# Optimization experiments

Measured on AMD Instinct MI355X. Metric: run time of the kernel, lower is better.

Reference implementation:

```python
import jax, jax.numpy as jnp
import numpy as np

B, S, HID = 4, 2048, 1024
NH, IM, E = 4, 2048, 4
EPS = 1e-6


def setup_inputs() -> dict:
    key = jax.random.key(0)
    ks = jax.random.split(key, 12)
    init = lambda k, shape: (jax.random.normal(k, shape, jnp.float32) * 0.02)
    return {
        "hidden_states": jax.random.normal(ks[0], (B, S, HID), jnp.float32),
        "ln1_w": jnp.ones((HID,), jnp.float32),
        "wq": init(ks[1], (HID, HID)),
        "wk": init(ks[2], (HID, HID)),
        "wv": init(ks[3], (HID, HID)),
        "wo": init(ks[4], (HID, HID)),
        "ln2_w": jnp.ones((HID,), jnp.float32),
        "router_w": init(ks[5], (HID, E)),
        "router_b": jnp.zeros((E,), jnp.float32),
        "gate_w": init(ks[6], (E, HID, IM)),
        "up_w": init(ks[7], (E, HID, IM)),
        "down_w": init(ks[8], (E, IM, HID)),
    }


def _rms(x, w):
    return w * (x * jax.lax.rsqrt(jnp.mean(x * x, axis=-1, keepdims=True) + EPS))


def reference(hidden_states, ln1_w, wq, wk, wv, wo, ln2_w,
              router_w, router_b, gate_w, up_w, down_w):
    b, s, h = hidden_states.shape
    nh, d = NH, h // NH

    # ---- attention block (elu+1 feature map, then full softmax) ----
    x = _rms(hidden_states, ln1_w)
    q = (x @ wq).reshape(b, s, nh, d).transpose(0, 2, 1, 3)  # [b,nh,s,d]
    k = (x @ wk).reshape(b, s, nh, d).transpose(0, 2, 1, 3)
    v = (x @ wv).reshape(b, s, nh, d).transpose(0, 2, 1, 3)
    q = jax.nn.elu(q) + 1.0
    k = jax.nn.elu(k) + 1.0
    scores = jnp.einsum('bhqd,bhkd->bhqk', q, k)
    attn = jax.nn.softmax(scores, axis=-1)  # dropout is identity at eval
    o = jnp.einsum('bhqk,bhkd->bhqd', attn, v)
    o = o.transpose(0, 2, 1, 3).reshape(b, s, h) @ wo
    h1 = hidden_states + o

    # ---- MoE block: router softmax, balance loss, dense expert loop ----
    x2 = _rms(h1, ln2_w)
    logits = x2 @ router_w + router_b            # [b,s,E]
    rw = jax.nn.softmax(logits, axis=-1)
    mean_routing = rw.mean(axis=0)               # mean over batch dim only, [s,E]
    balance_loss = jnp.mean((mean_routing - 1.0 / E) ** 2) * 0.01

    # source computes EVERY expert over all tokens, weighted by the FULL
    # softmax routing weight (top-k weights are computed but unused)
    moe_out = jnp.zeros_like(x2)
    for i in range(E):
        g = jax.nn.silu(x2 @ gate_w[i])
        u = x2 @ up_w[i]
        moe_out = moe_out + ((g * u) @ down_w[i]) * rw[..., i:i + 1]

    return h1 + moe_out, balance_loss
```

## Files before the change

### kernel.cpp

```cpp
#include <hip/hip_runtime.h>
#include <cstdint>
#include <cstddef>

#define B_    4
#define S_    2048
#define HID_  1024
#define NH_   4
#define HD_   256
#define IM_   2048
#define E_    4
#define M_    8192
#define NHG_  4

typedef __bf16 bf16x8 __attribute__((ext_vector_type(8)));
typedef float  f32x4  __attribute__((ext_vector_type(4)));

__device__ __forceinline__ unsigned short f32_to_bf16(float f) {
  unsigned int u = __float_as_uint(f);
  u += 0x7fffu + ((u >> 16) & 1u);
  return (unsigned short)(u >> 16);
}

__device__ __forceinline__ void gload16(const unsigned short* g, unsigned short* l) {
  __builtin_amdgcn_global_load_lds(
      (const __attribute__((address_space(1))) void*)g,
      (__attribute__((address_space(3))) void*)l, 16, 0, 0);
}

template<int N> __device__ __forceinline__ void vwait() {
  if constexpr (N == 0)      asm volatile("s_waitcnt vmcnt(0)" ::: "memory");
  else if constexpr (N == 2) asm volatile("s_waitcnt vmcnt(2)" ::: "memory");
  else if constexpr (N == 6) asm volatile("s_waitcnt vmcnt(6)" ::: "memory");
  else                       asm volatile("s_waitcnt vmcnt(8)" ::: "memory");
}
__device__ __forceinline__ void lgk0() {
  asm volatile("s_waitcnt lgkmcnt(0)" ::: "memory");
}

__device__ __forceinline__ void swizzle_xy(int& bx, int& by) {
  const int gx = gridDim.x, gy = gridDim.y;
  const int flat = blockIdx.x + blockIdx.y * gx;
  const int xcd = flat & 7, i = flat >> 3;
  const int rpx = gy >> 3;
  bx = i % gx;
  by = xcd * rpx + i / gx;
}

#define EPI_F32      0
#define EPI_VT       2
#define EPI_PV_O     3
#define EPI_WO       4
#define EPI_DOWN     5

struct EpiAux {
  float* c_f32;
  unsigned short* c_bf16;
  const float* add_src;
  float* out2;
  long long strideCz;
  int ldc;
};

template<int EPI>
__global__ __launch_bounds__(256) void gemm_bf16k(
    const unsigned short* __restrict__ A, int lda, long long sAo, long long sAi, int zbA,
    const unsigned short* __restrict__ B, int ldb, long long sBo, long long sBi, int zbB,
    int zshift, int zmask, int zbC, int K, EpiAux aux)
{
  __shared__ unsigned short As[2][128 * 32];
  __shared__ unsigned short Bs[2][128 * 32];

  const int t = threadIdx.x;
  int bx, by;
  swizzle_xy(bx, by);
  const int m0 = by * 128, n0 = bx * 128;
  const int z  = blockIdx.z;
  const int zA = z + zbA, zB = z + zbB, zC = z + zbC;
  const unsigned short* Ab = A + (long long)(zA >> zshift) * sAo + (long long)(zA & zmask) * sAi;
  const unsigned short* Bb = B + (long long)(zB >> zshift) * sBo + (long long)(zB & zmask) * sBi;

  const int lane = t & 63, wave = t >> 6;
  const int wm = (wave >> 1) * 64, wn = (wave & 1) * 64;
  const int lrow = lane & 15, quad = lane >> 4;

  f32x4 acc[4][4] = {};

  const int srow = lane >> 2;
  const int sko  = (lane & 3) * 8;
  const unsigned short* aRow0 = Ab + (long long)(m0 + wave * 16       + srow) * lda + sko;
  const unsigned short* aRow1 = Ab + (long long)(m0 + (wave + 4) * 16 + srow) * lda + sko;
  const unsigned short* bRow0 = Bb + (long long)(n0 + wave * 16       + srow) * ldb + sko;
  const unsigned short* bRow1 = Bb + (long long)(n0 + (wave + 4) * 16 + srow) * ldb + sko;
  const int dst0 = (wave * 16) * 32, dst1 = ((wave + 4) * 16) * 32;

  gload16(aRow0, &As[0][dst0]);
  gload16(aRow1, &As[0][dst1]);
  gload16(bRow0, &Bs[0][dst0]);
  gload16(bRow1, &Bs[0][dst1]);

  int cur = 0;
  for (int kk = 0; kk < K; kk += 32, cur ^= 1) {
    __syncthreads();
    if (kk + 32 < K) {
      const int nxt = cur ^ 1, k2 = kk + 32;
      gload16(aRow0 + k2, &As[nxt][dst0]);
      gload16(aRow1 + k2, &As[nxt][dst1]);
      gload16(bRow0 + k2, &Bs[nxt][dst0]);
      gload16(bRow1 + k2, &Bs[nxt][dst1]);
    }
    bf16x8 af[4], bfr[4];
    #pragma unroll
    for (int i = 0; i < 4; ++i) {
      af[i]  = *reinterpret_cast<const bf16x8*>(&As[cur][(wm + i * 16 + lrow) * 32 + quad * 8]);
      bfr[i] = *reinterpret_cast<const bf16x8*>(&Bs[cur][(wn + i * 16 + lrow) * 32 + quad * 8]);
    }
    #pragma unroll
    for (int i = 0; i < 4; ++i)
      #pragma unroll
      for (int j = 0; j < 4; ++j)
        acc[i][j] = __builtin_amdgcn_mfma_f32_16x16x32_bf16(af[i], bfr[j], acc[i][j], 0, 0, 0);
  }

  #pragma unroll
  for (int mi = 0; mi < 4; ++mi) {
    #pragma unroll
    for (int ni = 0; ni < 4; ++ni) {
      #pragma unroll
      for (int r = 0; r < 4; ++r) {
        const int gm = m0 + wm + mi * 16 + quad * 4 + r;
        const int gn = n0 + wn + ni * 16 + lrow;
        const float val = acc[mi][ni][r];
        if (EPI == EPI_F32) {
          aux.c_f32[(long long)zC * aux.strideCz + (long long)gm * aux.ldc + gn] = val;
        } else if (EPI == EPI_VT) {
          const int b = gm >> 11, s = gm & (S_ - 1);
          const int h = gn >> 8, d = gn & (HD_ - 1);
          aux.c_bf16[((long long)(b * NH_ + h) * HD_ + d) * S_ + s] = f32_to_bf16(val);
        } else if (EPI == EPI_PV_O) {
          const int b = zC >> 2, h = zC & (NH_ - 1);
          aux.c_bf16[((long long)(b * S_ + gm)) * HID_ + h * HD_ + gn] = f32_to_bf16(val);
        } else if (EPI == EPI_WO) {
          const long long idx = (long long)gm * HID_ + gn;
          aux.out2[idx] = val + aux.add_src[idx];
        } else if (EPI == EPI_DOWN) {
          const long long idx = (long long)gm * HID_ + gn;
          aux.out2[idx] += val;
        }
      }
    }
  }
}

#define EPI2_GU 1

template<int EPI2>
__global__ __launch_bounds__(256, 2) void gemm_dual_k(
    const unsigned short* __restrict__ A,
    const unsigned short* __restrict__ B0b,
    const unsigned short* __restrict__ B1b,
    int zb,
    unsigned short* __restrict__ out0, unsigned short* __restrict__ out1,
    const float* __restrict__ rw)
{
  __shared__ unsigned short As[2][128 * 32];
  __shared__ unsigned short B0s[2][128 * 32];
  __shared__ unsigned short B1s[2][128 * 32];

  const int t = threadIdx.x;
  int bx, by;
  swizzle_xy(bx, by);
  const int m0 = by * 128, n0 = bx * 128;

  const int lane = t & 63, wave = t >> 6;
  const int wm = (wave >> 1) * 64, wn = (wave & 1) * 64;
  const int lrow = lane & 15, quad = lane >> 4;

  f32x4 acc0[4][4] = {}, acc1[4][4] = {};

  const int srow = lane >> 2;
  const int sko  = (lane & 3) * 8;
  const unsigned short* aRow0 = A   + (long long)(m0 + wave * 16       + srow) * HID_ + sko;
  const unsigned short* aRow1 = A   + (long long)(m0 + (wave + 4) * 16 + srow) * HID_ + sko;
  const unsigned short* gRow0 = B0b + (long long)(n0 + wave * 16       + srow) * HID_ + sko;
  const unsigned short* gRow1 = B0b + (long long)(n0 + (wave + 4) * 16 + srow) * HID_ + sko;
  const unsigned short* uRow0 = B1b + (long long)(n0 + wave * 16       + srow) * HID_ + sko;
  const unsigned short* uRow1 = B1b + (long long)(n0 + (wave + 4) * 16 + srow) * HID_ + sko;
  const int dst0 = (wave * 16) * 32, dst1 = ((wave + 4) * 16) * 32;

  gload16(aRow0, &As[0][dst0]);
  gload16(aRow1, &As[0][dst1]);
  gload16(gRow0, &B0s[0][dst0]);
  gload16(gRow1, &B0s[0][dst1]);
  gload16(uRow0, &B1s[0][dst0]);
  gload16(uRow1, &B1s[0][dst1]);

  int cur = 0;
  for (int kk = 0; kk < HID_; kk += 32, cur ^= 1) {
    __syncthreads();
    if (kk + 32 < HID_) {
      const int nxt = cur ^ 1, k2 = kk + 32;
      gload16(aRow0 + k2, &As[nxt][dst0]);
      gload16(aRow1 + k2, &As[nxt][dst1]);
      gload16(gRow0 + k2, &B0s[nxt][dst0]);
      gload16(gRow1 + k2, &B0s[nxt][dst1]);
      gload16(uRow0 + k2, &B1s[nxt][dst0]);
      gload16(uRow1 + k2, &B1s[nxt][dst1]);
    }
    bf16x8 af[4], b0[4], b1[4];
    #pragma unroll
    for (int i = 0; i < 4; ++i) {
      af[i] = *reinterpret_cast<const bf16x8*>(&As[cur][(wm + i * 16 + lrow) * 32 + quad * 8]);
      b0[i] = *reinterpret_cast<const bf16x8*>(&B0s[cur][(wn + i * 16 + lrow) * 32 + quad * 8]);
      b1[i] = *reinterpret_cast<const bf16x8*>(&B1s[cur][(wn + i * 16 + lrow) * 32 + quad * 8]);
    }
    #pragma unroll
    for (int i = 0; i < 4; ++i)
      #pragma unroll
      for (int j = 0; j < 4; ++j) {
        acc0[i][j] = __builtin_amdgcn_mfma_f32_16x16x32_bf16(af[i], b0[j], acc0[i][j], 0, 0, 0);
        acc1[i][j] = __builtin_amdgcn_mfma_f32_16x16x32_bf16(af[i], b1[j], acc1[i][j], 0, 0, 0);
      }
  }

  #pragma unroll
  for (int mi = 0; mi < 4; ++mi)
    #pragma unroll
    for (int r = 0; r < 4; ++r) {
      const int gm = m0 + wm + mi * 16 + quad * 4 + r;
      const float rwv = rw[(long long)gm * E_ + zb];
      #pragma unroll
      for (int ni = 0; ni < 4; ++ni) {
        const int gn = n0 + wn + ni * 16 + lrow;
        const float v0 = acc0[mi][ni][r];
        const float v1 = acc1[mi][ni][r];
        const float sg = v0 / (1.f + __expf(-v0));
        out0[(long long)gm * IM_ + gn] = f32_to_bf16(sg * v1 * rwv);
      }
    }
}

#define EPI5_GU   0
#define EPI5_QK   1
#define EPI5_DOWN 2
#define EPI5_WO   3
template<bool DUAL, int EPI, int KTOT, int KROW, bool PAIRK>
__global__ __launch_bounds__(512, 2) void gemm5_k(
    const unsigned short* A0, const unsigned short* A1,
    const unsigned short* B0b, const unsigned short* B1b,
    const float* __restrict__ rw, int expert,
    unsigned short* out0, unsigned short* out1,
    float* o_f32, const float* add_src)
{
  constexpr int NT  = KTOT / 64;
  constexpr int NT2 = NT / 2;
  __shared__ unsigned short smem[DUAL ? 65536 : 57344];

  const int t = threadIdx.x, wave = t >> 6, lane = t & 63;
  const int lrow = lane & 15, quad = lane >> 4;
  const int wrow0 = (wave >> 1) * 64;
  const int wcol0 = (wave & 1) * 64;

  int bx, by;
  swizzle_xy(bx, by);
  const int m0 = by * 256, n0 = bx * 128;

  const int r8  = lane >> 3;
  const int csw = ((lane & 7) ^ r8) << 4;

  auto unit = [&](const unsigned short* mat, int grow0, int ktl, int ldsElem) {
    #pragma unroll
    for (int i = 0; i < 2; ++i) {
      const char* src = (const char*)(mat + (size_t)(grow0 + wave * 16 + i * 8 + r8) * KROW)
                        + (size_t)ktl * 128 + csw;
      gload16((const unsigned short*)src, &smem[ldsElem + wave * 1024 + i * 512]);
    }
  };
  auto stageA = [&](int kt) {
    const unsigned short* m = A0; int ktl = kt;
    if constexpr (PAIRK) { if (kt >= NT2) { m = A1; ktl = kt - NT2; } }
    const int buf = kt & 1;
    unit(m, m0,       ktl, buf * 16384);
    unit(m, m0 + 128, ktl, buf * 16384 + 8192);
  };
  auto stageB = [&](int kt, int which, int bufB) {
    const unsigned short* m; int ktl = kt;
    if constexpr (DUAL) {
      m = which ? B1b : B0b;
    } else {
      m = B0b;
      if constexpr (PAIRK) { if (kt >= NT2) { m = B1b; ktl = kt - NT2; } }
    }
    unit(m, n0, ktl, 32768 + (DUAL ? which * 16384 : 0) + bufB * 8192);
  };

  const int xr = (lane & 7) << 4;
  auto readA_ = [&](bf16x8* o, int buf, int ks) {
    const char* base = (const char*)smem + buf * 32768 + (wrow0 >> 7) * 16384;
    const int rl0 = wrow0 & 127;
    #pragma unroll
    for (int mi = 0; mi < 4; ++mi)
      o[mi] = *(const bf16x8*)(base + (rl0 + mi * 16 + lrow) * 128 + ((ks * 64 + quad * 16) ^ xr));
  };
  auto readB_ = [&](bf16x8* o, int baseByte, int ks) {
    const char* base = (const char*)smem + baseByte;
    #pragma unroll
    for (int nj = 0; nj < 4; ++nj)
      o[nj] = *(const bf16x8*)(base + (wcol0 + nj * 16 + lrow) * 128 + ((ks * 64 + quad * 16) ^ xr));
  };

  f32x4 acc0[4][4] = {};
  f32x4 acc1[4][4] = {};
  auto mm = [&](f32x4 (&ac)[4][4], const bf16x8* aF, const bf16x8* bF) {
    #pragma unroll
    for (int mi = 0; mi < 4; ++mi)
      #pragma unroll
      for (int nj = 0; nj < 4; ++nj)
        ac[mi][nj] = __builtin_amdgcn_mfma_f32_16x16x32_bf16(aF[mi], bF[nj], ac[mi][nj], 0, 0, 0);
  };

  bf16x8 a0[4], a1[4], bF[4];

  if constexpr (DUAL) {
    stageA(0); stageB(0, 1, 0); stageB(0, 0, 0); stageA(1); stageB(1, 1, 1);
    vwait<8>();
    __builtin_amdgcn_s_barrier();

    for (int T = 0; T < NT; ++T) {
      const int c = T & 1;
      const int bB1 = 65536 + 32768 + c * 16384;
      const int bB0 = 65536 + c * 16384;
      readA_(a0, c, 0);
      readB_(bF, bB1, 0);
      if (T + 1 < NT) stageB(T + 1, 0, (T + 1) & 1);
      if (T < NT - 1) vwait<8>(); else vwait<0>();
      __builtin_amdgcn_s_barrier();
      lgk0();
      __builtin_amdgcn_s_setprio(1); mm(acc1, a0, bF); __builtin_amdgcn_s_setprio(0);
      __builtin_amdgcn_s_barrier();
      readB_(bF, bB0, 0);
      __builtin_amdgcn_s_barrier();
      lgk0();
      __builtin_amdgcn_s_setprio(1); mm(acc0, a0, bF); __builtin_amdgcn_s_setprio(0);
      __builtin_amdgcn_s_barrier();
      readA_(a1, c, 1);
      readB_(bF, bB1, 1);
      __builtin_amdgcn_s_barrier();
      lgk0();
      __builtin_amdgcn_s_setprio(1); mm(acc1, a1, bF); __builtin_amdgcn_s_setprio(0);
      __builtin_amdgcn_s_barrier();
      readB_(bF, bB0, 1);
      if (T + 2 < NT) { stageA(T + 2); stageB(T + 2, 1, c); }
      if (T < NT - 2) vwait<8>();
      else if (T == NT - 2) vwait<2>();
      __builtin_amdgcn_s_barrier();
      lgk0();
      __builtin_amdgcn_s_setprio(1); mm(acc0, a1, bF); __builtin_amdgcn_s_setprio(0);
      __builtin_amdgcn_s_barrier();
    }
  } else {
    stageB(0, 0, 0); stageA(0); stageB(1, 0, 1); stageA(1);
    vwait<6>();
    __builtin_amdgcn_s_barrier();

    int b = 0;
    for (int T = 0; T < NT; ++T) {
      const int c = T & 1;
      const int bB = 65536 + b * 16384;
      int bn = b + 2; if (bn >= 3) bn -= 3;
      readA_(a0, c, 0);
      readA_(a1, c, 1);
      readB_(bF, bB, 0);
      if (T + 2 < NT) stageB(T + 2, 0, bn);
      __builtin_amdgcn_s_barrier();
      lgk0();
      __builtin_amdgcn_s_setprio(1); mm(acc0, a0, bF); __builtin_amdgcn_s_setprio(0);
      __builtin_amdgcn_s_barrier();
      readB_(bF, bB, 1);
      if (T + 2 < NT) stageA(T + 2);
      if (T < NT - 2) vwait<6>();
      else if (T == NT - 2) vwait<0>();
      __builtin_amdgcn_s_barrier();
      lgk0();
      __builtin_amdgcn_s_setprio(1); mm(acc0, a1, bF); __builtin_amdgcn_s_setprio(0);
      __builtin_amdgcn_s_barrier();
      if (++b == 3) b = 0;
    }
  }

  #pragma unroll
  for (int mi = 0; mi < 4; ++mi) {
    #pragma unroll
    for (int r = 0; r < 4; ++r) {
      const int gm = m0 + wrow0 + mi * 16 + quad * 4 + r;
      float rwv = 0.f;
      if (EPI == EPI5_GU) rwv = rw[(size_t)gm * E_ + expert];
      #pragma unroll
      for (int nj = 0; nj < 4; ++nj) {
        const int gn = n0 + wcol0 + nj * 16 + lrow;
        const float v0 = acc0[mi][nj][r];
        if (EPI == EPI5_GU) {
          const float v1 = acc1[mi][nj][r];
          const float sg = v0 / (1.f + __expf(-v0));
          out0[(size_t)gm * IM_ + gn] = f32_to_bf16(sg * v1 * rwv);
        } else if (EPI == EPI5_QK) {
          const float v1 = acc1[mi][nj][r];
          out0[(size_t)gm * HID_ + gn] = f32_to_bf16(v0 > 0.f ? v0 + 1.f : __expf(v0));
          out1[(size_t)gm * HID_ + gn] = f32_to_bf16(v1 > 0.f ? v1 + 1.f : __expf(v1));
        } else if (EPI == EPI5_DOWN) {
          o_f32[(size_t)gm * HID_ + gn] += v0;
        } else {
          const size_t idx = (size_t)gm * HID_ + gn;
          o_f32[idx] = v0 + add_src[idx];
        }
      }
    }
  }
}

__global__ void transpose_cast4_k(const float* s0, const float* s1,
                                  const float* s2, const float* s3,
                                  unsigned short* __restrict__ out, int R, int C)
{
  __shared__ float tile[32][33];
  const int z = blockIdx.z;
  const float* in = (z == 0) ? s0 : (z == 1) ? s1 : (z == 2) ? s2 : s3;
  unsigned short* o = out + (long long)z * R * C;
  const int c0 = blockIdx.x * 32, r0 = blockIdx.y * 32;
  const int tx = threadIdx.x, ty = threadIdx.y;
  #pragma unroll
  for (int i = 0; i < 32; i += 8)
    tile[ty + i][tx] = in[(long long)(r0 + ty + i) * C + c0 + tx];
  __syncthreads();
  #pragma unroll
  for (int i = 0; i < 32; i += 8)
    o[(long long)(c0 + ty + i) * R + r0 + tx] = f32_to_bf16(tile[tx][ty + i]);
}

__global__ void transpose_cast2x4_k(const float* __restrict__ sA,
                                    const float* __restrict__ sB,
                                    unsigned short* __restrict__ dA,
                                    unsigned short* __restrict__ dB,
                                    int R, int C)
{
  __shared__ float tile[32][33];
  const int z = blockIdx.z;
  const long long eo = (long long)(z & 3) * R * C;
  const float* in = ((z < 4) ? sA : sB) + eo;
  unsigned short* o = ((z < 4) ? dA : dB) + eo;
  const int c0 = blockIdx.x * 32, r0 = blockIdx.y * 32;
  const int tx = threadIdx.x, ty = threadIdx.y;
  #pragma unroll
  for (int i = 0; i < 32; i += 8)
    tile[ty + i][tx] = in[(long long)(r0 + ty + i) * C + c0 + tx];
  __syncthreads();
  #pragma unroll
  for (int i = 0; i < 32; i += 8)
    o[(long long)(c0 + ty + i) * R + r0 + tx] = f32_to_bf16(tile[tx][ty + i]);
}

__global__ void transpose_cast_k(const float* __restrict__ in,
                                 unsigned short* __restrict__ out, int R, int C)
{
  __shared__ float tile[32][33];
  const long long bo = (long long)blockIdx.z * R * C;
  const int c0 = blockIdx.x * 32, r0 = blockIdx.y * 32;
  const int tx = threadIdx.x, ty = threadIdx.y;
  #pragma unroll
  for (int i = 0; i < 32; i += 8)
    tile[ty + i][tx] = in[bo + (long long)(r0 + ty + i) * C + c0 + tx];
  __syncthreads();
  #pragma unroll
  for (int i = 0; i < 32; i += 8)
    out[bo + (long long)(c0 + ty + i) * R + r0 + tx] = f32_to_bf16(tile[tx][ty + i]);
}

__global__ __launch_bounds__(256) void rmsnorm_cast_k(
    const float* __restrict__ x, const float* __restrict__ w,
    unsigned short* __restrict__ out)
{
  __shared__ float red[4];
  const int row = blockIdx.x, t = threadIdx.x;
  const float4 v = reinterpret_cast<const float4*>(x + (long long)row * HID_)[t];
  float ss = v.x * v.x + v.y * v.y + v.z * v.z + v.w * v.w;
  #pragma unroll
  for (int off = 32; off > 0; off >>= 1) ss += __shfl_down(ss, off, 64);
  if ((t & 63) == 0) red[t >> 6] = ss;
  __syncthreads();
  ss = red[0] + red[1] + red[2] + red[3];
  const float inv = rsqrtf(ss * (1.0f / HID_) + 1e-6f);
  const float4 wv = reinterpret_cast<const float4*>(w)[t];
  ushort4 o;
  o.x = f32_to_bf16(v.x * inv * wv.x);
  o.y = f32_to_bf16(v.y * inv * wv.y);
  o.z = f32_to_bf16(v.z * inv * wv.z);
  o.w = f32_to_bf16(v.w * inv * wv.w);
  reinterpret_cast<ushort4*>(out + (long long)row * HID_)[t] = o;
}

__global__ __launch_bounds__(256) void softmax_rows_k(float* __restrict__ scores)
{
  __shared__ float red[4];
  const long long rbase = ((long long)blockIdx.y * S_ + blockIdx.x) * S_;
  float* row = scores + rbase;
  const int t = threadIdx.x;
  float v[8];
  #pragma unroll
  for (int i = 0; i < 8; ++i) v[i] = row[t + i * 256];
  float m = v[0];
  #pragma unroll
  for (int i = 1; i < 8; ++i) m = fmaxf(m, v[i]);
  #pragma unroll
  for (int off = 32; off > 0; off >>= 1) m = fmaxf(m, __shfl_down(m, off, 64));
  if ((t & 63) == 0) red[t >> 6] = m;
  __syncthreads();
  m = fmaxf(fmaxf(red[0], red[1]), fmaxf(red[2], red[3]));
  __syncthreads();
  float s = 0.f;
  #pragma unroll
  for (int i = 0; i < 8; ++i) { v[i] = __expf(v[i] - m); s += v[i]; }
  #pragma unroll
  for (int off = 32; off > 0; off >>= 1) s += __shfl_down(s, off, 64);
  if ((t & 63) == 0) red[t >> 6] = s;
  __syncthreads();
  const float inv = 1.0f / (red[0] + red[1] + red[2] + red[3]);
  unsigned short* prow = reinterpret_cast<unsigned short*>(scores) + rbase * 2;
  #pragma unroll
  for (int i = 0; i < 8; ++i) prow[t + i * 256] = f32_to_bf16(v[i] * inv);
}

__global__ __launch_bounds__(256) void router_k(
    const float* __restrict__ h1, const float* __restrict__ ln2w,
    const float* __restrict__ rwgt, const float* __restrict__ rbias,
    float* __restrict__ rw)
{
  const int wv = threadIdx.x >> 6, lane = threadIdx.x & 63;
  const long long m = (long long)blockIdx.x * 4 + wv;
  const float* xr = h1 + m * HID_;
  float xv[16];
  float ss = 0.f;
  #pragma unroll
  for (int i = 0; i < 16; ++i) { xv[i] = xr[lane + i * 64]; ss += xv[i] * xv[i]; }
  #pragma unroll
  for (int off = 32; off > 0; off >>= 1) ss += __shfl_down(ss, off, 64);
  ss = __shfl(ss, 0, 64);
  const float inv = rsqrtf(ss * (1.0f / HID_) + 1e-6f);
  float l0 = 0, l1 = 0, l2 = 0, l3 = 0;
  #pragma unroll
  for (int i = 0; i < 16; ++i) {
    const int k = lane + i * 64;
    const float xn = xv[i] * inv * ln2w[k];
    const float4 wr = reinterpret_cast<const float4*>(rwgt)[k];
    l0 += xn * wr.x; l1 += xn * wr.y; l2 += xn * wr.z; l3 += xn * wr.w;
  }
  #pragma unroll
  for (int off = 32; off > 0; off >>= 1) {
    l0 += __shfl_down(l0, off, 64);
    l1 += __shfl_down(l1, off, 64);
    l2 += __shfl_down(l2, off, 64);
    l3 += __shfl_down(l3, off, 64);
  }
  if (lane == 0) {
    l0 += rbias[0]; l1 += rbias[1]; l2 += rbias[2]; l3 += rbias[3];
    const float mx = fmaxf(fmaxf(l0, l1), fmaxf(l2, l3));
    const float e0 = __expf(l0 - mx), e1 = __expf(l1 - mx);
    const float e2 = __expf(l2 - mx), e3 = __expf(l3 - mx);
    const float is = 1.0f / (e0 + e1 + e2 + e3);
    reinterpret_cast<float4*>(rw)[m] = make_float4(e0 * is, e1 * is, e2 * is, e3 * is);
  }
}

__global__ __launch_bounds__(256) void balance_k(const float* __restrict__ rw,
                                                 float* __restrict__ out_scalar)
{
  __shared__ float red[4];
  float acc = 0.f;
  for (int it = threadIdx.x; it < S_ * E_; it += 256) {
    const int s = it >> 2, e = it & 3;
    float mr = 0.f;
    #pragma unroll
    for (int b = 0; b < B_; ++b) mr += rw[((long long)b * S_ + s) * E_ + e];
    mr *= (1.0f / B_);
    const float d = mr - 1.0f / E_;
    acc += d * d;
  }
  #pragma unroll
  for (int off = 32; off > 0; off >>= 1) acc += __shfl_down(acc, off, 64);
  if ((threadIdx.x & 63) == 0) red[threadIdx.x >> 6] = acc;
  __syncthreads();
  if (threadIdx.x == 0)
    out_scalar[0] = (red[0] + red[1] + red[2] + red[3]) * (0.01f / (S_ * E_));
}

extern "C" void kernel_launch(void* const* d_in, const int* in_sizes, int n_in,
                              void* d_out, int out_size, void* d_ws, size_t ws_size,
                              hipStream_t stream)
{
  const float* hidden   = (const float*)d_in[0];
  const float* ln1w     = (const float*)d_in[1];
  const float* wq       = (const float*)d_in[2];
  const float* wk       = (const float*)d_in[3];
  const float* wv       = (const float*)d_in[4];
  const float* wo       = (const float*)d_in[5];
  const float* ln2w     = (const float*)d_in[6];
  const float* router_w = (const float*)d_in[7];
  const float* router_b = (const float*)d_in[8];
  const float* gate_w   = (const float*)d_in[9];
  const float* up_w     = (const float*)d_in[10];
  const float* down_w   = (const float*)d_in[11];
  float* out = (float*)d_out;

  char* ws = (char*)d_ws;
  size_t off = 0;
  auto carve = [&](size_t bytes) {
    off = (off + 255) & ~(size_t)255;
    char* p = ws + off;
    off += bytes;
    return p;
  };
  unsigned short* wqT   = (unsigned short*)carve((size_t)HID_ * HID_ * 2);
  unsigned short* wkT   = (unsigned short*)carve((size_t)HID_ * HID_ * 2);
  unsigned short* wvT   = (unsigned short*)carve((size_t)HID_ * HID_ * 2);
  unsigned short* woT   = (unsigned short*)carve((size_t)HID_ * HID_ * 2);
  unsigned short* x_bf  = (unsigned short*)carve((size_t)M_ * HID_ * 2);
  unsigned short* qb    = (unsigned short*)carve((size_t)M_ * HID_ * 2);
  unsigned short* kb    = (unsigned short*)carve((size_t)M_ * HID_ * 2);
  unsigned short* vT    = (unsigned short*)carve((size_t)M_ * HID_ * 2);
  float*          rwbuf = (float*)carve((size_t)M_ * E_ * 4);
  char*           ubase = carve((size_t)NHG_ * S_ * S_ * 4);
  float*          scores = (float*)ubase;
  unsigned short* gateT = (unsigned short*)(ubase);
  unsigned short* upT   = (unsigned short*)(ubase + (size_t)16 * 1024 * 1024);
  unsigned short* downT = (unsigned short*)(ubase + (size_t)32 * 1024 * 1024);
  unsigned short* o_bf  = x_bf;
  unsigned short* x2_bf = qb;
  unsigned short* gu0   = kb;
  unsigned short* gu1   = (unsigned short*)carve((size_t)M_ * IM_ * 2);
  const bool paired = (ws_size >= off);

  const dim3 blk256(256), blk512(512), blkT(32, 8);

  transpose_cast4_k<<<dim3(32, 32, 4), blkT, 0, stream>>>(wq, wk, wv, wo, wqT, HID_, HID_);

  rmsnorm_cast_k<<<M_, blk256, 0, stream>>>(hidden, ln1w, x_bf);

  gemm5_k<true, EPI5_QK, 1024, 1024, false><<<dim3(8, 32, 1), blk512, 0, stream>>>(
      x_bf, nullptr, wqT, wkT, nullptr, 0, qb, kb, nullptr, nullptr);
  {
    EpiAux a{}; a.c_bf16 = vT;
    gemm_bf16k<EPI_VT><<<dim3(8, 64, 1), blk256, 0, stream>>>(
        x_bf, HID_, 0, 0, 0, wvT, HID_, 0, 0, 0, 0, 0, 0, HID_, a);
  }

  for (int grp = 0; grp < 16 / NHG_; ++grp) {
    EpiAux as{}; as.c_f32 = scores; as.ldc = S_; as.strideCz = (long long)S_ * S_;
    gemm_bf16k<EPI_F32><<<dim3(16, 16, NHG_), blk256, 0, stream>>>(
        qb, HID_, (long long)S_ * HID_, HD_, grp * NHG_,
        kb, HID_, (long long)S_ * HID_, HD_, grp * NHG_,
        2, 3, 0, HD_, as);
    softmax_rows_k<<<dim3(S_, NHG_, 1), blk256, 0, stream>>>(scores);
    EpiAux ap{}; ap.c_bf16 = o_bf;
    gemm_bf16k<EPI_PV_O><<<dim3(2, 16, NHG_), blk256, 0, stream>>>(
        (const unsigned short*)scores, 2 * S_, (long long)S_ * 2 * S_, 0, 0,
        vT, S_, (long long)HD_ * S_, 0, grp * NHG_,
        0, 0, grp * NHG_, S_, ap);
  }

  transpose_cast2x4_k<<<dim3(64, 32, 8), blkT, 0, stream>>>(
      gate_w, up_w, gateT, upT, HID_, IM_);
  transpose_cast_k<<<dim3(32, 64, E_), blkT, 0, stream>>>(down_w, downT, IM_, HID_);

  gemm5_k<false, EPI5_WO, 1024, 1024, false><<<dim3(8, 32, 1), blk512, 0, stream>>>(
      o_bf, nullptr, woT, nullptr, nullptr, 0, nullptr, nullptr, out, hidden);

  rmsnorm_cast_k<<<M_, blk256, 0, stream>>>(out, ln2w, x2_bf);
  router_k<<<M_ / 4, blk256, 0, stream>>>(out, ln2w, router_w, router_b, rwbuf);
  balance_k<<<1, blk256, 0, stream>>>(rwbuf, out + (size_t)M_ * HID_);

  const size_t wsz = (size_t)IM_ * HID_;
  if (paired) {
    for (int p = 0; p < 2; ++p) {
      const int e0 = 2 * p, e1 = e0 + 1;
      gemm5_k<true, EPI5_GU, 1024, 1024, false><<<dim3(16, 32, 1), blk512, 0, stream>>>(
          x2_bf, nullptr, gateT + (size_t)e0 * wsz, upT + (size_t)e0 * wsz,
          rwbuf, e0, gu0, nullptr, nullptr, nullptr);
      gemm5_k<true, EPI5_GU, 1024, 1024, false><<<dim3(16, 32, 1), blk512, 0, stream>>>(
          x2_bf, nullptr, gateT + (size_t)e1 * wsz, upT + (size_t)e1 * wsz,
          rwbuf, e1, gu1, nullptr, nullptr, nullptr);
      gemm5_k<false, EPI5_DOWN, 4096, 2048, true><<<dim3(8, 32, 1), blk512, 0, stream>>>(
          gu0, gu1, downT + (size_t)e0 * wsz, downT + (size_t)e1 * wsz,
          nullptr, 0, nullptr, nullptr, out, nullptr);
    }
  } else {
    for (int i = 0; i < E_; ++i) {
      gemm_dual_k<EPI2_GU><<<dim3(16, 64, 1), blk256, 0, stream>>>(
          x2_bf, gateT + (size_t)i * wsz, upT + (size_t)i * wsz, i, gu0, nullptr, rwbuf);
      EpiAux ad{}; ad.out2 = out;
      gemm_bf16k<EPI_DOWN><<<dim3(8, 64, 1), blk256, 0, stream>>>(
          gu0, IM_, 0, 0, 0, downT + (size_t)i * wsz, IM_, 0, 0, 0,
          0, 0, 0, IM_, ad);
    }
  }
}
```

Baseline: 1.082 ms.

## Restructure GEMM prefetch pipeline with precomputed pointers and triple-buffered A

Rewrites the main MFMA GEMM kernel's load schedule. Global source pointers and LDS read offsets are now precomputed and advanced incrementally rather than recomputed per stage. The dual kernel reorders its MFMA phases and splits its A/B prefetches across phases. The single-B path now triple-buffers both A and B, which adds LDS (the shared array grows) to keep more loads in flight and cut address arithmetic and stalls in the pipeline. The higher LDS use may reduce occupancy, and the waitcnt accounting is more delicate.

Result: no change. 1.074 ms (-0.7%).

```diff
diff --git a/kernel.cpp b/kernel.cpp
--- a/kernel.cpp
+++ b/kernel.cpp
@@ -30,6 +30,7 @@
 template<int N> __device__ __forceinline__ void vwait() {
   if constexpr (N == 0)      asm volatile("s_waitcnt vmcnt(0)" ::: "memory");
   else if constexpr (N == 2) asm volatile("s_waitcnt vmcnt(2)" ::: "memory");
+  else if constexpr (N == 4) asm volatile("s_waitcnt vmcnt(4)" ::: "memory");
   else if constexpr (N == 6) asm volatile("s_waitcnt vmcnt(6)" ::: "memory");
   else                       asm volatile("s_waitcnt vmcnt(8)" ::: "memory");
 }
@@ -244,7 +245,7 @@
 #define EPI5_DOWN 2
 #define EPI5_WO   3
 template<bool DUAL, int EPI, int KTOT, int KROW, bool PAIRK>
-__global__ __launch_bounds__(512, 2) void gemm5_k(
+__global__ __launch_bounds__(512, 2) void gemm6_k(
     const unsigned short* A0, const unsigned short* A1,
     const unsigned short* B0b, const unsigned short* B1b,
     const float* __restrict__ rw, int expert,
@@ -253,7 +254,7 @@
 {
   constexpr int NT  = KTOT / 64;
   constexpr int NT2 = NT / 2;
-  __shared__ unsigned short smem[DUAL ? 65536 : 57344];
+  __shared__ unsigned short smem[DUAL ? 65536 : 73728];
 
   const int t = threadIdx.x, wave = t >> 6, lane = t & 63;
   const int lrow = lane & 15, quad = lane >> 4;
@@ -267,123 +268,147 @@
   const int r8  = lane >> 3;
   const int csw = ((lane & 7) ^ r8) << 4;
 
-  auto unit = [&](const unsigned short* mat, int grow0, int ktl, int ldsElem) {
+  const char* pA[4]; const char* qA[4];
+  const char* pB0[2]; const char* pB1[2];
+  #pragma unroll
+  for (int h = 0; h < 2; ++h)
     #pragma unroll
     for (int i = 0; i < 2; ++i) {
-      const char* src = (const char*)(mat + (size_t)(grow0 + wave * 16 + i * 8 + r8) * KROW)
-                        + (size_t)ktl * 128 + csw;
-      gload16((const unsigned short*)src, &smem[ldsElem + wave * 1024 + i * 512]);
+      const int row = m0 + h * 128 + wave * 16 + i * 8 + r8;
+      pA[h * 2 + i] = (const char*)(A0 + (size_t)row * KROW) + csw;
+      if constexpr (PAIRK) qA[h * 2 + i] = (const char*)(A1 + (size_t)row * KROW) + csw;
+    }
+  #pragma unroll
+  for (int i = 0; i < 2; ++i) {
+    const int row = n0 + wave * 16 + i * 8 + r8;
+    pB0[i] = (const char*)(B0b + (size_t)row * KROW) + csw;
+    if constexpr (DUAL || PAIRK) pB1[i] = (const char*)(B1b + (size_t)row * KROW) + csw;
+  }
+
+  const int dAe[4] = { wave * 1024, wave * 1024 + 512,
+                       8192 + wave * 1024, 8192 + wave * 1024 + 512 };
+  const int dBe[2] = { wave * 1024, wave * 1024 + 512 };
+
+  auto stA_h = [&](int h, int bufAel) {
+    #pragma unroll
+    for (int i = 0; i < 2; ++i) {
+      const int j = h * 2 + i;
+      gload16((const unsigned short*)pA[j], &smem[bufAel + dAe[j]]);
+      pA[j] += 128;
     }
   };
-  auto stageA = [&](int kt) {
-    const unsigned short* m = A0; int ktl = kt;
-    if constexpr (PAIRK) { if (kt >= NT2) { m = A1; ktl = kt - NT2; } }
-    const int buf = kt & 1;
-    unit(m, m0,       ktl, buf * 16384);
-    unit(m, m0 + 128, ktl, buf * 16384 + 8192);
+  auto stB_ = [&](const char** pB, int bel) {
+    #pragma unroll
+    for (int i = 0; i < 2; ++i) {
+      gload16((const unsigned short*)pB[i], &smem[bel + dBe[i]]);
+      pB[i] += 128;
+    }
   };
-  auto stageB = [&](int kt, int which, int bufB) {
-    const unsigned short* m; int ktl = kt;
-    if constexpr (DUAL) {
-      m = which ? B1b : B0b;
-    } else {
-      m = B0b;
-      if constexpr (PAIRK) { if (kt >= NT2) { m = B1b; ktl = kt - NT2; } }
-    }
-    unit(m, n0, ktl, 32768 + (DUAL ? which * 16384 : 0) + bufB * 8192);
+
+  const int xr = (lane & 7) << 4;
+  int roA[4], roB[4];
+  #pragma unroll
+  for (int mi = 0; mi < 4; ++mi)
+    roA[mi] = (wrow0 >> 7) * 16384 + ((wrow0 & 64) + mi * 16 + lrow) * 128
+              + ((quad * 16) ^ xr);
+  #pragma unroll
+  for (int nj = 0; nj < 4; ++nj)
+    roB[nj] = (wcol0 + nj * 16 + lrow) * 128 + ((quad * 16) ^ xr);
+
+  auto readA_ = [&](bf16x8* o, int aByte, int ks) {
+    const char* base = (const char*)smem + aByte;
+    #pragma unroll
+    for (int mi = 0; mi < 4; ++mi)
+      o[mi] = *(const bf16x8*)(base + (roA[mi] ^ (ks * 64)));
   };
-
-  const int xr = (lane & 7) << 4;
-  auto readA_ = [&](bf16x8* o, int buf, int ks) {
-    const char* base = (const char*)smem + buf * 32768 + (wrow0 >> 7) * 16384;
-    const int rl0 = wrow0 & 127;
-    #pragma unroll
-    for (int mi = 0; mi < 4; ++mi)
-      o[mi] = *(const bf16x8*)(base + (rl0 + mi * 16 + lrow) * 128 + ((ks * 64 + quad * 16) ^ xr));
-  };
-  auto readB_ = [&](bf16x8* o, int baseByte, int ks) {
-    const char* base = (const char*)smem + baseByte;
+  auto readB_ = [&](bf16x8* o, int bByte, int ks) {
+    const char* base = (const char*)smem + bByte;
     #pragma unroll
     for (int nj = 0; nj < 4; ++nj)
-      o[nj] = *(const bf16x8*)(base + (wcol0 + nj * 16 + lrow) * 128 + ((ks * 64 + quad * 16) ^ xr));
+      o[nj] = *(const bf16x8*)(base + (roB[nj] ^ (ks * 64)));
   };
 
   f32x4 acc0[4][4] = {};
   f32x4 acc1[4][4] = {};
-  auto mm = [&](f32x4 (&ac)[4][4], const bf16x8* aF, const bf16x8* bF) {
+  auto mm = [&](f32x4 (&ac)[4][4], const bf16x8* aF, const bf16x8* bFr) {
     #pragma unroll
     for (int mi = 0; mi < 4; ++mi)
       #pragma unroll
       for (int nj = 0; nj < 4; ++nj)
-        ac[mi][nj] = __builtin_amdgcn_mfma_f32_16x16x32_bf16(aF[mi], bF[nj], ac[mi][nj], 0, 0, 0);
+        ac[mi][nj] = __builtin_amdgcn_mfma_f32_16x16x32_bf16(aF[mi], bFr[nj], ac[mi][nj], 0, 0, 0);
   };
 
   bf16x8 a0[4], a1[4], bF[4];
 
   if constexpr (DUAL) {
-    stageA(0); stageB(0, 1, 0); stageB(0, 0, 0); stageA(1); stageB(1, 1, 1);
-    vwait<8>();
+    stA_h(0, 0); stA_h(1, 0);
+    stB_(pB0, 32768); stB_(pB1, 49152);
+    stA_h(0, 16384); stA_h(1, 16384);
+    vwait<4>();
     __builtin_amdgcn_s_barrier();
 
     for (int T = 0; T < NT; ++T) {
-      const int c = T & 1;
-      const int bB1 = 65536 + 32768 + c * 16384;
-      const int bB0 = 65536 + c * 16384;
-      readA_(a0, c, 0);
-      readB_(bF, bB1, 0);
-      if (T + 1 < NT) stageB(T + 1, 0, (T + 1) & 1);
-      if (T < NT - 1) vwait<8>(); else vwait<0>();
+      const int c = T & 1, cn = c ^ 1;
+      const int aB  = c * 32768;
+      const int b0B = 65536 + c * 16384;
+      const int b1B = 98304 + c * 16384;
+      readA_(a0, aB, 0); readB_(bF, b0B, 0);
+      if (T + 1 < NT) stB_(pB0, 32768 + cn * 8192);
+      __builtin_amdgcn_s_barrier();
+      lgk0();
+      __builtin_amdgcn_s_setprio(1); mm(acc0, a0, bF); __builtin_amdgcn_s_setprio(0);
+      __builtin_amdgcn_s_barrier();
+      readA_(a1, aB, 1); readB_(bF, b0B, 1);
+      if (T + 1 < NT) stB_(pB1, 49152 + cn * 8192);
+      __builtin_amdgcn_s_barrier();
+      lgk0();
+      __builtin_amdgcn_s_setprio(1); mm(acc0, a1, bF); __builtin_amdgcn_s_setprio(0);
+      __builtin_amdgcn_s_barrier();
+      readB_(bF, b1B, 0);
+      if (T + 2 < NT) stA_h(0, c * 16384);
       __builtin_amdgcn_s_barrier();
       lgk0();
       __builtin_amdgcn_s_setprio(1); mm(acc1, a0, bF); __builtin_amdgcn_s_setprio(0);
       __builtin_amdgcn_s_barrier();
-      readB_(bF, bB0, 0);
+      readB_(bF, b1B, 1);
+      if (T + 2 < NT) { stA_h(1, c * 16384); vwait<4>(); }
+      else            { vwait<0>(); }
+      __builtin_amdgcn_s_barrier();
+      lgk0();
+      __builtin_amdgcn_s_setprio(1); mm(acc1, a1, bF); __builtin_amdgcn_s_setprio(0);
+      __builtin_amdgcn_s_barrier();
+    }
+  } else {
+    stB_(pB0, 49152); stA_h(0, 0); stA_h(1, 0);
+    stB_(pB0, 49152 + 8192); stA_h(0, 16384); stA_h(1, 16384);
+    vwait<6>();
+    __builtin_amdgcn_s_barrier();
+
+    int ab = 0, tg = 2;
+    for (int T = 0; T < NT; ++T) {
+      const int aB = ab * 32768;
+      const int bB = 98304 + ab * 16384;
+      const int aT = tg * 16384;
+      const int bT = 49152 + tg * 8192;
+      readA_(a0, aB, 0); readB_(bF, bB, 0);
+      if (PAIRK && T + 2 == NT2) {
+        pB0[0] = pB1[0]; pB0[1] = pB1[1];
+        pA[0] = qA[0]; pA[1] = qA[1]; pA[2] = qA[2]; pA[3] = qA[3];
+      }
+      if (T + 2 < NT) { stB_(pB0, bT); stA_h(0, aT); }
       __builtin_amdgcn_s_barrier();
       lgk0();
       __builtin_amdgcn_s_setprio(1); mm(acc0, a0, bF); __builtin_amdgcn_s_setprio(0);
       __builtin_amdgcn_s_barrier();
-      readA_(a1, c, 1);
-      readB_(bF, bB1, 1);
-      __builtin_amdgcn_s_barrier();
-      lgk0();
-      __builtin_amdgcn_s_setprio(1); mm(acc1, a1, bF); __builtin_amdgcn_s_setprio(0);
-      __builtin_amdgcn_s_barrier();
-      readB_(bF, bB0, 1);
-      if (T + 2 < NT) { stageA(T + 2); stageB(T + 2, 1, c); }
-      if (T < NT - 2) vwait<8>();
-      else if (T == NT - 2) vwait<2>();
+      readA_(a1, aB, 1); readB_(bF, bB, 1);
+      if (T + 2 < NT) { stA_h(1, aT); vwait<6>(); }
+      else            { vwait<0>(); }
       __builtin_amdgcn_s_barrier();
       lgk0();
       __builtin_amdgcn_s_setprio(1); mm(acc0, a1, bF); __builtin_amdgcn_s_setprio(0);
       __builtin_amdgcn_s_barrier();
-    }
-  } else {
-    stageB(0, 0, 0); stageA(0); stageB(1, 0, 1); stageA(1);
-    vwait<6>();
-    __builtin_amdgcn_s_barrier();
-
-    int b = 0;
-    for (int T = 0; T < NT; ++T) {
-      const int c = T & 1;
-      const int bB = 65536 + b * 16384;
-      int bn = b + 2; if (bn >= 3) bn -= 3;
-      readA_(a0, c, 0);
-      readA_(a1, c, 1);
-      readB_(bF, bB, 0);
-      if (T + 2 < NT) stageB(T + 2, 0, bn);
-      __builtin_amdgcn_s_barrier();
-      lgk0();
-      __builtin_amdgcn_s_setprio(1); mm(acc0, a0, bF); __builtin_amdgcn_s_setprio(0);
-      __builtin_amdgcn_s_barrier();
-      readB_(bF, bB, 1);
-      if (T + 2 < NT) stageA(T + 2);
-      if (T < NT - 2) vwait<6>();
-      else if (T == NT - 2) vwait<0>();
-      __builtin_amdgcn_s_barrier();
-      lgk0();
-      __builtin_amdgcn_s_setprio(1); mm(acc0, a1, bF); __builtin_amdgcn_s_setprio(0);
-      __builtin_amdgcn_s_barrier();
-      if (++b == 3) b = 0;
+      if (++ab == 3) ab = 0;
+      if (++tg == 3) tg = 0;
     }
   }
 
@@ -643,7 +668,7 @@
 
   rmsnorm_cast_k<<<M_, blk256, 0, stream>>>(hidden, ln1w, x_bf);
 
-  gemm5_k<true, EPI5_QK, 1024, 1024, false><<<dim3(8, 32, 1), blk512, 0, stream>>>(
+  gemm6_k<true, EPI5_QK, 1024, 1024, false><<<dim3(8, 32, 1), blk512, 0, stream>>>(
       x_bf, nullptr, wqT, wkT, nullptr, 0, qb, kb, nullptr, nullptr);
   {
     EpiAux a{}; a.c_bf16 = vT;
@@ -669,7 +694,7 @@
       gate_w, up_w, gateT, upT, HID_, IM_);
   transpose_cast_k<<<dim3(32, 64, E_), blkT, 0, stream>>>(down_w, downT, IM_, HID_);
 
-  gemm5_k<false, EPI5_WO, 1024, 1024, false><<<dim3(8, 32, 1), blk512, 0, stream>>>(
+  gemm6_k<false, EPI5_WO, 1024, 1024, false><<<dim3(8, 32, 1), blk512, 0, stream>>>(
       o_bf, nullptr, woT, nullptr, nullptr, 0, nullptr, nullptr, out, hidden);
 
   rmsnorm_cast_k<<<M_, blk256, 0, stream>>>(out, ln2w, x2_bf);
@@ -680,13 +705,13 @@
   if (paired) {
     for (int p = 0; p < 2; ++p) {
       const int e0 = 2 * p, e1 = e0 + 1;
-      gemm5_k<true, EPI5_GU, 1024, 1024, false><<<dim3(16, 32, 1), blk512, 0, stream>>>(
+      gemm6_k<true, EPI5_GU, 1024, 1024, false><<<dim3(16, 32, 1), blk512, 0, stream>>>(
           x2_bf, nullptr, gateT + (size_t)e0 * wsz, upT + (size_t)e0 * wsz,
           rwbuf, e0, gu0, nullptr, nullptr, nullptr);
-      gemm5_k<true, EPI5_GU, 1024, 1024, false><<<dim3(16, 32, 1), blk512, 0, stream>>>(
+      gemm6_k<true, EPI5_GU, 1024, 1024, false><<<dim3(16, 32, 1), blk512, 0, stream>>>(
           x2_bf, nullptr, gateT + (size_t)e1 * wsz, upT + (size_t)e1 * wsz,
           rwbuf, e1, gu1, nullptr, nullptr, nullptr);
-      gemm5_k<false, EPI5_DOWN, 4096, 2048, true><<<dim3(8, 32, 1), blk512, 0, stream>>>(
+      gemm6_k<false, EPI5_DOWN, 4096, 2048, true><<<dim3(8, 32, 1), blk512, 0, stream>>>(
           gu0, gu1, downT + (size_t)e0 * wsz, downT + (size_t)e1 * wsz,
           nullptr, 0, nullptr, nullptr, out, nullptr);
     }
```
